# Kernel tuning notes

Hardware: AMD Instinct MI355X
Metric: run time of the kernel (lower is better)

The kernel has to match this reference:

```python
import jax, jax.numpy as jnp
import numpy as np

N_LEVELS = 127.0  # 2^(8-1)-1, symmetric signed int8


def _ste_round_clip(x, scale, lo, hi):
    """Fake-quantize x to integers in [lo,hi] at given scale, straight-through estimator."""
    q = jnp.clip(jnp.round(x / scale), lo, hi) * scale
    return x + jax.lax.stop_gradient(q - x)


def quant_act(x):
    """Per-tensor symmetric int8 activation quantization (QuantAct)."""
    scale = jax.lax.stop_gradient(jnp.max(jnp.abs(x)) / N_LEVELS)
    xq = _ste_round_clip(x, scale, -N_LEVELS - 1.0, N_LEVELS)
    return xq, scale


def quant_linear(xq, act_scale, w, b):
    """Per-tensor symmetric int8 weight quantization + bias quantized at act*weight scale (QuantLinear)."""
    w_scale = jax.lax.stop_gradient(jnp.max(jnp.abs(w)) / N_LEVELS)
    wq = _ste_round_clip(w, w_scale, -N_LEVELS, N_LEVELS)
    bias_scale = act_scale * w_scale
    bq = b + jax.lax.stop_gradient(jnp.round(b / bias_scale) * bias_scale - b)
    out = xq @ wq.T + bq  # equivalent to int8 GEMM accumulated in int32, dequantized
    return out, w_scale


def setup_inputs() -> dict:
    key = jax.random.key(0)
    ks = jax.random.split(key, 7)
    B, D_IN, D_H, D_OUT = 512, 9216, 4096, 1000  # AlexNet head dims
    s1 = 1.0 / np.sqrt(D_IN)
    s2 = 1.0 / np.sqrt(D_H)
    return {
        "x": jax.random.normal(ks[0], (B, D_IN), jnp.float32),
        "w1": jax.random.normal(ks[1], (D_H, D_IN), jnp.float32) * s1,
        "b1": jax.random.normal(ks[2], (D_H,), jnp.float32) * 0.01,
        "w2": jax.random.normal(ks[3], (D_H, D_H), jnp.float32) * s2,
        "b2": jax.random.normal(ks[4], (D_H,), jnp.float32) * 0.01,
        "w3": jax.random.normal(ks[5], (D_OUT, D_H), jnp.float32) * s2,
        "b3": jax.random.normal(ks[6], (D_OUT,), jnp.float32) * 0.01,
    }


def reference(x, w1, b1, w2, b2, w3, b3):
    # quant_act -> quant_fc1 -> ReLU -> (Dropout: eval=identity) -> quant_act1 -> quant_fc2 -> ReLU -> quant_act2 -> quant_fc3
    xq, a_s = quant_act(x)
    h, _ = quant_linear(xq, a_s, w1, b1)
    h = jax.nn.relu(h)
    hq, a_s = quant_act(h)
    h, _ = quant_linear(hq, a_s, w2, b2)
    h = jax.nn.relu(h)
    hq, a_s = quant_act(h)
    out, _ = quant_linear(hq, a_s, w3, b3)
    return out
```

## Files before the change

kernel.cpp:

```cpp
#include <hip/hip_runtime.h>
#include <hip/hip_bf16.h>

typedef __attribute__((ext_vector_type(4))) int   int32x4;
typedef __attribute__((ext_vector_type(4))) float float4v;


__global__ void init_stats(float* stats) {
    if (threadIdx.x < 64) stats[threadIdx.x] = 0.0f;
}

__global__ void maxabs_kernel(const float* __restrict__ src, long nchunk, float* __restrict__ out) {
    const int tid  = threadIdx.x;
    const int lane = tid & 63;
    const int wid  = tid >> 6;
    __shared__ float red[4];
    float m0 = 0.0f, m1 = 0.0f, m2 = 0.0f, m3 = 0.0f;
    for (long c = blockIdx.x; c < nchunk; c += gridDim.x) {
        const float4v* p = (const float4v*)src + c * 1024 + tid;
        float4v v0 = p[0], v1 = p[256], v2 = p[512], v3 = p[768];
        m0 = fmaxf(m0, fmaxf(fmaxf(fabsf(v0.x), fabsf(v0.y)), fmaxf(fabsf(v0.z), fabsf(v0.w))));
        m1 = fmaxf(m1, fmaxf(fmaxf(fabsf(v1.x), fabsf(v1.y)), fmaxf(fabsf(v1.z), fabsf(v1.w))));
        m2 = fmaxf(m2, fmaxf(fmaxf(fabsf(v2.x), fabsf(v2.y)), fmaxf(fabsf(v2.z), fabsf(v2.w))));
        m3 = fmaxf(m3, fmaxf(fmaxf(fabsf(v3.x), fabsf(v3.y)), fmaxf(fabsf(v3.z), fabsf(v3.w))));
    }
    float m = fmaxf(fmaxf(m0, m1), fmaxf(m2, m3));
    #pragma unroll
    for (int off = 32; off; off >>= 1) m = fmaxf(m, __shfl_xor(m, off, 64));
    if (lane == 0) red[wid] = m;
    __syncthreads();
    if (tid == 0) {
        float r = fmaxf(fmaxf(red[0], red[1]), fmaxf(red[2], red[3]));
        atomicMax((unsigned int*)out, __float_as_uint(r));
    }
}

__global__ void quant_kernel(const float* __restrict__ src, signed char* __restrict__ dst,
                             const float* __restrict__ stats, int slot,
                             float lo, float hi, long nchunk) {
    const float scale = stats[slot] / 127.0f;
    const int tid = threadIdx.x;
    for (long c = blockIdx.x; c < nchunk; c += gridDim.x) {
        const float4v* p = (const float4v*)src + c * 1024 + tid;
        int* d = (int*)dst + c * 1024 + tid;
        float4v v0 = p[0], v1 = p[256], v2 = p[512], v3 = p[768];
        float4v vs[4] = {v0, v1, v2, v3};
        int packed[4];
        #pragma unroll
        for (int j = 0; j < 4; ++j) {
            float4v v = vs[j];
            int b0 = (int)fminf(fmaxf(rintf(v.x / scale), lo), hi);
            int b1 = (int)fminf(fmaxf(rintf(v.y / scale), lo), hi);
            int b2 = (int)fminf(fmaxf(rintf(v.z / scale), lo), hi);
            int b3 = (int)fminf(fmaxf(rintf(v.w / scale), lo), hi);
            packed[j] = (b0 & 0xff) | ((b1 & 0xff) << 8) | ((b2 & 0xff) << 16) | ((b3 & 0xff) << 24);
        }
        d[0]   = packed[0];
        d[256] = packed[1];
        d[512] = packed[2];
        d[768] = packed[3];
    }
}

template <int BM, int BN, int FR, int FC, bool RELUMAX>
__global__ __launch_bounds__(256, 4)
void gemm_q8(const signed char* __restrict__ A, const signed char* __restrict__ Bw,
             const float* __restrict__ bias, float* __restrict__ stats,
             int a_slot, int w_slot, int h_slot,
             float* __restrict__ C, int K, int Ncols) {
    constexpr int BK = 64;
    constexpr int NWC = BN / (FC * 16);
    static_assert((BM / (FR * 16)) * (BN / (FC * 16)) == 4, "4 waves");
    constexpr int LDS_A = BM * BK;
    constexpr int LDS_TILE = (BM + BN) * BK;
    __shared__ __align__(16) signed char lds[2][LDS_TILE];

    const int tid  = threadIdx.x;
    const int wid  = tid >> 6;
    const int lane = tid & 63;
    const int wr   = wid / NWC;
    const int wc   = wid % NWC;

    const long brow = (long)blockIdx.y * BM;
    const long bcol = (long)blockIdx.x * BN;

    const signed char* Ab = A  + brow * K;
    const signed char* Bb = Bw + bcol * K;

    const int srow = tid >> 2;
    const int scb  = (tid & 3) * 16;

    int32x4 zero = {0, 0, 0, 0};
    int32x4 acc[FR][FC];
    #pragma unroll
    for (int r = 0; r < FR; ++r)
        #pragma unroll
        for (int c = 0; c < FC; ++c) acc[r][c] = zero;

    auto stage = [&](int buf, int kt) {
        #pragma unroll
        for (int i = 0; i < BM / 64; ++i) {
            __builtin_amdgcn_global_load_lds(
                (const __attribute__((address_space(1))) void*)(Ab + (long)(srow + i * 64) * K + kt + scb),
                (__attribute__((address_space(3))) void*)(&lds[buf][(srow + i * 64) * BK + scb]),
                16, 0, 0);
        }
        #pragma unroll
        for (int i = 0; i < BN / 64; ++i) {
            __builtin_amdgcn_global_load_lds(
                (const __attribute__((address_space(1))) void*)(Bb + (long)(srow + i * 64) * K + kt + scb),
                (__attribute__((address_space(3))) void*)(&lds[buf][LDS_A + (srow + i * 64) * BK + scb]),
                16, 0, 0);
        }
    };

    const int nt = K / BK;
    stage(0, 0);
    __syncthreads();

    int cur = 0;
    for (int t = 0; t < nt; ++t) {
        if (t + 1 < nt) stage(cur ^ 1, (t + 1) * BK);

        const signed char* la = &lds[cur][0];
        const signed char* lb = &lds[cur][LDS_A];
        int32x4 af[FR], bf[FC];
        #pragma unroll
        for (int r = 0; r < FR; ++r)
            af[r] = *(const int32x4*)(la + (wr * (FR * 16) + r * 16 + (lane & 15)) * BK + (lane >> 4) * 16);
        #pragma unroll
        for (int c = 0; c < FC; ++c)
            bf[c] = *(const int32x4*)(lb + (wc * (FC * 16) + c * 16 + (lane & 15)) * BK + (lane >> 4) * 16);

        #pragma unroll
        for (int r = 0; r < FR; ++r)
            #pragma unroll
            for (int c = 0; c < FC; ++c)
                acc[r][c] = __builtin_amdgcn_mfma_i32_16x16x64_i8(af[r], bf[c], acc[r][c], 0, 0, 0);

        __syncthreads();
        cur ^= 1;
    }

    const float sa = stats[a_slot] / 127.0f;
    const float sw = stats[w_slot] / 127.0f;
    const float s  = sa * sw;
    float lmax = 0.0f;
    #pragma unroll
    for (int c = 0; c < FC; ++c) {
        const long col = bcol + wc * (FC * 16) + c * 16 + (lane & 15);
        const bool colok = (col < Ncols);
        float bint = 0.0f;
        if (colok) bint = rintf(bias[col] / s);
        #pragma unroll
        for (int r = 0; r < FR; ++r) {
            #pragma unroll
            for (int j = 0; j < 4; ++j) {
                const long row = brow + wr * (FR * 16) + r * 16 + (lane >> 4) * 4 + j;
                float v = ((float)acc[r][c][j] + bint) * s;
                if (RELUMAX) v = fmaxf(v, 0.0f);
                if (colok) C[row * Ncols + col] = v;
                if (RELUMAX) lmax = fmaxf(lmax, v);
            }
        }
    }
    if (RELUMAX) {
        __shared__ float red[4];
        #pragma unroll
        for (int off = 32; off; off >>= 1) lmax = fmaxf(lmax, __shfl_xor(lmax, off, 64));
        if (lane == 0) red[wid] = lmax;
        __syncthreads();
        if (tid == 0) {
            float r = fmaxf(fmaxf(red[0], red[1]), fmaxf(red[2], red[3]));
            atomicMax((unsigned int*)&stats[h_slot], __float_as_uint(r));
        }
    }
}

static inline long lminl(long a, long b) { return a < b ? a : b; }

extern "C" void kernel_launch(void* const* d_in, const int* in_sizes, int n_in,
                              void* d_out, int out_size, void* d_ws, size_t ws_size,
                              hipStream_t stream) {
    const float* x  = (const float*)d_in[0];
    const float* w1 = (const float*)d_in[1];
    const float* b1 = (const float*)d_in[2];
    const float* w2 = (const float*)d_in[3];
    const float* b2 = (const float*)d_in[4];
    const float* w3 = (const float*)d_in[5];
    const float* b3 = (const float*)d_in[6];
    float* out = (float*)d_out;

    constexpr int B = 512, DIN = 9216, DH = 4096, DOUT = 1000;

    char* ws = (char*)d_ws;
    float*       stats = (float*)ws;
    signed char* xq    = (signed char*)(ws + 256);
    signed char* w1q   = xq  + (size_t)B * DIN;
    signed char* w2q   = w1q + (size_t)DH * DIN;
    signed char* w3q   = w2q + (size_t)DH * DH;
    signed char* h1q   = w3q + (size_t)1024 * DH;
    signed char* h2q   = h1q + (size_t)B * DH;
    float*       hbuf  = (float*)(h2q + (size_t)B * DH);
    const size_t need  = 256 + (size_t)B*DIN + (size_t)DH*DIN + (size_t)DH*DH + (size_t)1024*DH
                       + 2*(size_t)B*DH + (size_t)B*DH*4;
    if (ws_size < need) return;

    init_stats<<<1, 64, 0, stream>>>(stats);

    auto launch_maxabs = [&](const float* p, long n, int slot) {
        long nchunk = n / 4096;
        int blocks = (int)lminl(nchunk, 2048);
        maxabs_kernel<<<blocks, 256, 0, stream>>>(p, nchunk, stats + slot);
    };
    auto launch_quant = [&](const float* p, signed char* q, long n, int slot, float lo) {
        long nchunk = n / 4096;
        int blocks = (int)lminl(nchunk, 2048);
        quant_kernel<<<blocks, 256, 0, stream>>>(p, q, stats, slot, lo, 127.0f, nchunk);
    };

    launch_maxabs(x, (long)B * DIN, 0);
    launch_quant(x, xq, (long)B * DIN, 0, -128.0f);
    launch_maxabs(w1, (long)DH * DIN, 1);
    launch_quant(w1, w1q, (long)DH * DIN, 1, -127.0f);
    launch_maxabs(w2, (long)DH * DH, 2);
    launch_quant(w2, w2q, (long)DH * DH, 2, -127.0f);
    launch_maxabs(w3, (long)DOUT * DH, 3);
    launch_quant(w3, w3q, (long)DOUT * DH, 3, -127.0f);

    gemm_q8<64, 128, 2, 4, true><<<dim3(DH / 128, B / 64), 256, 0, stream>>>(
        xq, w1q, b1, stats, 0, 1, 4, hbuf, DIN, DH);
    launch_quant(hbuf, h1q, (long)B * DH, 4, -128.0f);

    gemm_q8<64, 128, 2, 4, true><<<dim3(DH / 128, B / 64), 256, 0, stream>>>(
        h1q, w2q, b2, stats, 4, 2, 5, hbuf, DH, DH);
    launch_quant(hbuf, h2q, (long)B * DH, 5, -128.0f);

    gemm_q8<64, 64, 2, 2, false><<<dim3(16, B / 64), 256, 0, stream>>>(
        h2q, w3q, b3, stats, 5, 3, 0, out, DH, DOUT);
}
```

Baseline: 543.0 us.

## Triple-buffer int8 GEMM LDS with vmcnt waits and XOR swizzle

Moves the int8 GEMM main loop from double to triple buffering. Tiles are prefetched two steps ahead and synchronised with a single s_waitcnt vmcnt(L)+barrier per iteration, replacing two __syncthreads. An XOR swizzle is applied to the global source column of the direct-to-LDS loads and matched in the fragment reads, to reduce LDS bank conflicts. Launch bounds drop to 2 blocks per CU to fit the larger LDS footprint, which can lower occupancy.

```diff
diff --git a/kernel.cpp b/kernel.cpp
--- a/kernel.cpp
+++ b/kernel.cpp
@@ -62,17 +62,18 @@
 }
 
 template <int BM, int BN, int FR, int FC, bool RELUMAX>
-__global__ __launch_bounds__(256, 4)
+__global__ __launch_bounds__(256, 2)
 void gemm_q8(const signed char* __restrict__ A, const signed char* __restrict__ Bw,
              const float* __restrict__ bias, float* __restrict__ stats,
              int a_slot, int w_slot, int h_slot,
              float* __restrict__ C, int K, int Ncols) {
     constexpr int BK = 64;
     constexpr int NWC = BN / (FC * 16);
+    constexpr int L = BM / 64 + BN / 64;
     static_assert((BM / (FR * 16)) * (BN / (FC * 16)) == 4, "4 waves");
     constexpr int LDS_A = BM * BK;
     constexpr int LDS_TILE = (BM + BN) * BK;
-    __shared__ __align__(16) signed char lds[2][LDS_TILE];
+    __shared__ __align__(16) signed char lds[3][LDS_TILE];
 
     const int tid  = threadIdx.x;
     const int wid  = tid >> 6;
@@ -88,6 +89,7 @@
 
     const int srow = tid >> 2;
     const int scb  = (tid & 3) * 16;
+    const int scsrc = scb ^ (((srow >> 1) & 3) << 4);
 
     int32x4 zero = {0, 0, 0, 0};
     int32x4 acc[FR][FC];
@@ -100,14 +102,14 @@
         #pragma unroll
         for (int i = 0; i < BM / 64; ++i) {
             __builtin_amdgcn_global_load_lds(
-                (const __attribute__((address_space(1))) void*)(Ab + (long)(srow + i * 64) * K + kt + scb),
+                (const __attribute__((address_space(1))) void*)(Ab + (long)(srow + i * 64) * K + kt + scsrc),
                 (__attribute__((address_space(3))) void*)(&lds[buf][(srow + i * 64) * BK + scb]),
                 16, 0, 0);
         }
         #pragma unroll
         for (int i = 0; i < BN / 64; ++i) {
             __builtin_amdgcn_global_load_lds(
-                (const __attribute__((address_space(1))) void*)(Bb + (long)(srow + i * 64) * K + kt + scb),
+                (const __attribute__((address_space(1))) void*)(Bb + (long)(srow + i * 64) * K + kt + scsrc),
                 (__attribute__((address_space(3))) void*)(&lds[buf][LDS_A + (srow + i * 64) * BK + scb]),
                 16, 0, 0);
         }
@@ -115,30 +117,37 @@
 
     const int nt = K / BK;
     stage(0, 0);
-    __syncthreads();
-
-    int cur = 0;
+    if (nt > 1) stage(1, BK);
+
     for (int t = 0; t < nt; ++t) {
-        if (t + 1 < nt) stage(cur ^ 1, (t + 1) * BK);
-
-        const signed char* la = &lds[cur][0];
-        const signed char* lb = &lds[cur][LDS_A];
+        if (t + 1 < nt) {
+            asm volatile("s_waitcnt vmcnt(%0)\n\ts_barrier" :: "n"(L) : "memory");
+        } else {
+            asm volatile("s_waitcnt vmcnt(0)\n\ts_barrier" ::: "memory");
+        }
+        if (t + 2 < nt) stage((t + 2) % 3, (t + 2) * BK);
+
+        const signed char* la = &lds[t % 3][0];
+        const signed char* lb = &lds[t % 3][LDS_A];
         int32x4 af[FR], bf[FC];
         #pragma unroll
-        for (int r = 0; r < FR; ++r)
-            af[r] = *(const int32x4*)(la + (wr * (FR * 16) + r * 16 + (lane & 15)) * BK + (lane >> 4) * 16);
-        #pragma unroll
-        for (int c = 0; c < FC; ++c)
-            bf[c] = *(const int32x4*)(lb + (wc * (FC * 16) + c * 16 + (lane & 15)) * BK + (lane >> 4) * 16);
+        for (int r = 0; r < FR; ++r) {
+            const int row = wr * (FR * 16) + r * 16 + (lane & 15);
+            const int col = ((lane >> 4) * 16) ^ (((row >> 1) & 3) << 4);
+            af[r] = *(const int32x4*)(la + row * BK + col);
+        }
+        #pragma unroll
+        for (int c = 0; c < FC; ++c) {
+            const int row = wc * (FC * 16) + c * 16 + (lane & 15);
+            const int col = ((lane >> 4) * 16) ^ (((row >> 1) & 3) << 4);
+            bf[c] = *(const int32x4*)(lb + row * BK + col);
+        }
 
         #pragma unroll
         for (int r = 0; r < FR; ++r)
             #pragma unroll
             for (int c = 0; c < FC; ++c)
                 acc[r][c] = __builtin_amdgcn_mfma_i32_16x16x64_i8(af[r], bf[c], acc[r][c], 0, 0, 0);
-
-        __syncthreads();
-        cur ^= 1;
     }
 
     const float sa = stats[a_slot] / 127.0f;
```

Result: no change. 545.0 us (+0.4%).
